# Kernel optimization log

Measured on AMD Instinct MI355X. Metric: run time of the kernel, lower is better.

The kernel has to match this reference:

```python
import jax, jax.numpy as jnp
import numpy as np

B, S, D = 2, 1024, 1024
N_HEADS = 16
R = 128
M = 8
N_NEURONS = 256


def group_gate(gate, n_basis):
    # gate: [B,S,N] -> [B,S,M], sum over consecutive groups, then normalize
    b, s, n = gate.shape
    gs = n // n_basis  # exact by construction (256/8)
    g = gate.reshape(b, s, n_basis, gs).sum(axis=-1)
    return g / (g.sum(axis=-1, keepdims=True) + 1e-8)


def feature_fn(x, neurons, weights):
    # x:[B,S,D], neurons:[M,D,R], weights:[B,S,M] -> h:[B,S,R]
    all_h = jnp.einsum('bsd,mdr->bsmr', x, neurons)
    return jnp.einsum('bsmr,bsm->bsr', all_h, weights)


def restore_fn(h, neurons, weights):
    # h:[B,S,R], neurons:[M,R,D], weights:[B,S,M] -> [B,S,D]
    pre = jnp.einsum('bsr,bsm->bsmr', h, weights)
    return jnp.einsum('bsmr,mrd->bsd', pre, neurons)


def setup_inputs() -> dict:
    key = jax.random.key(0)
    ks = jax.random.split(key, 9)
    sc = 0.02
    return {
        'x': jax.random.normal(ks[0], (B, S, D), jnp.float32),
        'qk_f': jax.random.normal(ks[1], (M, D, R), jnp.float32) * sc,
        'qk_r': jax.random.normal(ks[2], (M, R, D), jnp.float32) * sc,
        'v_f': jax.random.normal(ks[3], (M, D, R), jnp.float32) * sc,
        'v_r': jax.random.normal(ks[4], (M, R, D), jnp.float32) * sc,
        'Wg_q': jax.random.normal(ks[5], (D, N_NEURONS), jnp.float32) * sc,
        'Wg_k': jax.random.normal(ks[6], (D, N_NEURONS), jnp.float32) * sc,
        'Wg_v': jax.random.normal(ks[7], (D, N_NEURONS), jnp.float32) * sc,
        'W_O': jax.random.normal(ks[8], (D, D), jnp.float32) * sc,
    }


def reference(x, qk_f, qk_r, v_f, v_r, Wg_q, Wg_k, Wg_v, W_O):
    # Router gates (softmax over neuron dim), then grouped per basis
    g_Q = jax.nn.softmax(jnp.einsum('bsd,dn->bsn', x, Wg_q), axis=-1)
    g_K = jax.nn.softmax(jnp.einsum('bsd,dn->bsn', x, Wg_k), axis=-1)
    g_V = jax.nn.softmax(jnp.einsum('bsd,dn->bsn', x, Wg_v), axis=-1)
    gQ_b = group_gate(g_Q, M)
    gK_b = group_gate(g_K, M)
    gV_b = group_gate(g_V, M)

    Q = restore_fn(feature_fn(x, qk_f, gQ_b), qk_r, gQ_b)
    K = restore_fn(feature_fn(x, qk_f, gK_b), qk_r, gK_b)
    V = restore_fn(feature_fn(x, v_f, gV_b), v_r, gV_b)

    d_head = D // N_HEADS
    Q = Q.reshape(B, S, N_HEADS, d_head).transpose(0, 2, 1, 3)
    K = K.reshape(B, S, N_HEADS, d_head).transpose(0, 2, 1, 3)
    V = V.reshape(B, S, N_HEADS, d_head).transpose(0, 2, 1, 3)

    scale = jnp.sqrt(jnp.float32(d_head))
    scores = jnp.einsum('bhsd,bhtd->bhst', Q, K) / scale
    causal = jnp.tril(jnp.ones((S, S), dtype=jnp.bool_))
    scores = jnp.where(causal, scores, jnp.finfo(scores.dtype).min)
    attn_w = jax.nn.softmax(scores, axis=-1)
    out = jnp.einsum('bhst,bhtd->bhsd', attn_w, V)
    out = out.transpose(0, 2, 1, 3).reshape(B, S, D)
    out = jnp.einsum('bsd,de->bse', out, W_O)
    return out
```

## Files before the change

### kernel.cpp

```cpp
#include <hip/hip_runtime.h>
#include <hip/hip_bf16.h>

#define BB 2
#define SS 1024
#define DD 1024
#define NH 16
#define DH 64
#define MM 8
#define RR 128
#define NN 256
#define NT (BB*SS)

using bf16 = __hip_bfloat16;

typedef __attribute__((ext_vector_type(8))) short short8;
typedef __attribute__((ext_vector_type(4))) short short4v;
typedef __attribute__((ext_vector_type(4))) float f32x4;

#define EXP2F(x) __builtin_amdgcn_exp2f(x)

#define GLD16(g, l) __builtin_amdgcn_global_load_lds( \
    (const __attribute__((address_space(1))) void*)(g), \
    (__attribute__((address_space(3))) void*)(l), 16, 0, 0)

__device__ __forceinline__ short8 lds_load8(const short* p) {
    short4v a = *(const short4v*)p;
    short4v b = *(const short4v*)(p + 4);
    short8 r;
    r[0] = a[0]; r[1] = a[1]; r[2] = a[2]; r[3] = a[3];
    r[4] = b[0]; r[5] = b[1]; r[6] = b[2]; r[7] = b[3];
    return r;
}

template <int NR>
__device__ __forceinline__ void stage_tile(const bf16* __restrict__ src, int k0,
                                           bf16* lds, int wave, int lane) {
#pragma unroll
    for (int i = 0; i < NR / 32; ++i) {
        const int L = i * 256 + wave * 64 + lane;
        const int row = L >> 3;
        const int gch = (L & 7) ^ ((row >> 1) & 7);
        GLD16(src + (size_t)row * DD + k0 + gch * 8, &lds[(i * 256 + wave * 64) * 8]);
    }
}

__device__ __forceinline__ short8 fragld(const bf16* lds, int rc, int kk, int quad) {
    int slot = (kk * 4 + quad) ^ ((rc >> 1) & 7);
    return *(const short8*)&((const short*)lds)[(rc * 8 + slot) * 8];
}

__device__ __forceinline__ void gemm128_pipe1(
    const bf16* __restrict__ A, const bf16* __restrict__ Bt, bf16* __restrict__ C,
    int Nz, int m0, int n0, bf16* As, bf16* Bs,
    int wave, int lane, int quad, int l15) {
    const int wr = wave >> 1, wc = wave & 1;
    f32x4 acc[4][4];
#pragma unroll
    for (int i = 0; i < 4; ++i)
#pragma unroll
        for (int j = 0; j < 4; ++j) acc[i][j] = (f32x4)0.f;

    const bf16* Ab = A + (size_t)m0 * DD;
    const bf16* Bb = Bt + (size_t)n0 * DD;

    stage_tile<128>(Ab, 0, As, wave, lane);
    stage_tile<128>(Bb, 0, Bs, wave, lane);
    __syncthreads();

    for (int it = 0; it < 16; ++it) {
        const int buf = it & 1;
        const bf16* Asc = As + buf * 8192;
        const bf16* Bsc = Bs + buf * 8192;
        if (it < 15) {
            stage_tile<128>(Ab, (it + 1) * 64, As + (buf ^ 1) * 8192, wave, lane);
            stage_tile<128>(Bb, (it + 1) * 64, Bs + (buf ^ 1) * 8192, wave, lane);
        }
#pragma unroll
        for (int kk = 0; kk < 2; ++kk) {
            short8 aF[4], bF[4];
#pragma unroll
            for (int bi = 0; bi < 4; ++bi) aF[bi] = fragld(Asc, wr * 64 + bi * 16 + l15, kk, quad);
#pragma unroll
            for (int bj = 0; bj < 4; ++bj) bF[bj] = fragld(Bsc, wc * 64 + bj * 16 + l15, kk, quad);
#pragma unroll
            for (int bi = 0; bi < 4; ++bi)
#pragma unroll
                for (int bj = 0; bj < 4; ++bj)
                    acc[bi][bj] = __builtin_amdgcn_mfma_f32_16x16x32_bf16(aF[bi], bF[bj], acc[bi][bj], 0, 0, 0);
        }
        __syncthreads();
    }

#pragma unroll
    for (int bi = 0; bi < 4; ++bi)
#pragma unroll
        for (int bj = 0; bj < 4; ++bj)
#pragma unroll
            for (int r = 0; r < 4; ++r) {
                int row = m0 + wr * 64 + bi * 16 + quad * 4 + r;
                int col = n0 + wc * 64 + bj * 16 + l15;
                C[(size_t)row * Nz + col] = __float2bfloat16(acc[bi][bj][r]);
            }
}

struct ProjArgs {
    const bf16 *xb, *f0, *f1, *wg;
    bf16 *allh0, *allh1, *lg;
    const float* csrc[3];
    bf16* cdst[3];
};

__global__ __launch_bounds__(256, 2) void mfma_proj(ProjArgs P) {
    __shared__ __align__(16) char smem[65536];
    const int bidx = blockIdx.x;
    const int tid = threadIdx.x;

    if (bidx >= 352) {
        float (*tile)[33] = (float(*)[33])smem;
        const int cb = bidx - 352;
        const int j = cb >> 10;
        const int t = cb & 1023;
        const int kb = t >> 5, rb = t & 31;
        const int tx = tid & 31, ty0 = tid >> 5;
        const float* s = P.csrc[j] + ((size_t)(kb * 32) * 1024) + rb * 32 + tx;
#pragma unroll
        for (int p = 0; p < 4; ++p)
            tile[ty0 + p * 8][tx] = s[(size_t)(ty0 + p * 8) * 1024];
        __syncthreads();
        bf16* dd = P.cdst[j] + ((size_t)(rb * 32) * 1024) + kb * 32 + tx;
#pragma unroll
        for (int p = 0; p < 4; ++p)
            dd[(size_t)(ty0 + p * 8) * 1024] = __float2bfloat16(tile[tx][ty0 + p * 8]);
        return;
    }

    bf16* As = (bf16*)smem;
    bf16* Bs = As + 2 * 128 * 64;
    const int wave = tid >> 6, lane = tid & 63;
    const int quad = lane >> 4, l15 = lane & 15;
    const int wk = (bidx & 7) * 44 + (bidx >> 3);
    if (wk < 256) {
        const int z = wk >> 7;
        const int r = wk & 127;
        gemm128_pipe1(P.xb, z ? P.f1 : P.f0, z ? P.allh1 : P.allh0, 1024,
                      (r >> 3) * 128, (r & 7) * 128, As, Bs, wave, lane, quad, l15);
    } else {
        const int r = wk - 256;
        gemm128_pipe1(P.xb, P.wg, P.lg, 768, (r / 6) * 128, (r % 6) * 128,
                      As, Bs, wave, lane, quad, l15);
    }
}

struct RestZ {
    const bf16* A[3];
    const bf16* Bt[3];
    bf16* C[3];
};

__global__ __launch_bounds__(256, 2) void mfma_restore(RestZ R) {
    __shared__ __align__(16) char smem[65536];
    bf16* As = (bf16*)smem;
    bf16* Bs = As + 2 * 128 * 64;
    const int tid = threadIdx.x;
    const int wave = tid >> 6, lane = tid & 63;
    const int quad = lane >> 4, l15 = lane & 15;
    const int wk = (blockIdx.x & 7) * 48 + (blockIdx.x >> 3);
    const int z = wk >> 7;
    const int r = wk & 127;
    gemm128_pipe1(R.A[z], R.Bt[z], R.C[z], DD, (r >> 3) * 128, (r & 7) * 128,
                  As, Bs, wave, lane, quad, l15);
}

__global__ __launch_bounds__(256, 3) void mfma_wo(
    const bf16* __restrict__ A, const bf16* __restrict__ Bt, float* __restrict__ C) {
    __shared__ __align__(16) bf16 As[3 * 64 * 64];
    __shared__ __align__(16) bf16 Bs[3 * 64 * 64];
    const int tid = threadIdx.x;
    const int wave = tid >> 6, lane = tid & 63;
    const int quad = lane >> 4, l15 = lane & 15;
    const int wr = wave >> 1, wc = wave & 1;
    const int wk = (blockIdx.x & 7) * 64 + (blockIdx.x >> 3);
    const int m0 = (wk >> 4) * 64, n0 = (wk & 15) * 64;

    f32x4 acc[2][2];
#pragma unroll
    for (int i = 0; i < 2; ++i)
#pragma unroll
        for (int j = 0; j < 2; ++j) acc[i][j] = (f32x4)0.f;

    const bf16* Ab = A + (size_t)m0 * DD;
    const bf16* Bb = Bt + (size_t)n0 * DD;

    stage_tile<64>(Ab, 0, As, wave, lane);
    stage_tile<64>(Bb, 0, Bs, wave, lane);
    stage_tile<64>(Ab, 64, As + 4096, wave, lane);
    stage_tile<64>(Bb, 64, Bs + 4096, wave, lane);

    int cur = 0;
    for (int it = 0; it < 16; ++it) {
        const int k0 = it * 64;
        int nxt = cur + 2; if (nxt >= 3) nxt -= 3;
        if (it < 14) {
            stage_tile<64>(Ab, k0 + 128, As + nxt * 4096, wave, lane);
            stage_tile<64>(Bb, k0 + 128, Bs + nxt * 4096, wave, lane);
            asm volatile("s_waitcnt vmcnt(8)" ::: "memory");
        } else if (it == 14) {
            asm volatile("s_waitcnt vmcnt(4)" ::: "memory");
        } else {
            asm volatile("s_waitcnt vmcnt(0)" ::: "memory");
        }
        __builtin_amdgcn_s_barrier();

        const bf16* Asc = As + cur * 4096;
        const bf16* Bsc = Bs + cur * 4096;
#pragma unroll
        for (int kk = 0; kk < 2; ++kk) {
            short8 aF[2], bF[2];
#pragma unroll
            for (int bi = 0; bi < 2; ++bi) aF[bi] = fragld(Asc, wr * 32 + bi * 16 + l15, kk, quad);
#pragma unroll
            for (int bj = 0; bj < 2; ++bj) bF[bj] = fragld(Bsc, wc * 32 + bj * 16 + l15, kk, quad);
#pragma unroll
            for (int bi = 0; bi < 2; ++bi)
#pragma unroll
                for (int bj = 0; bj < 2; ++bj)
                    acc[bi][bj] = __builtin_amdgcn_mfma_f32_16x16x32_bf16(aF[bi], bF[bj], acc[bi][bj], 0, 0, 0);
        }
        __builtin_amdgcn_s_barrier();
        cur = cur + 1; if (cur == 3) cur = 0;
    }
#pragma unroll
    for (int bi = 0; bi < 2; ++bi)
#pragma unroll
        for (int bj = 0; bj < 2; ++bj)
#pragma unroll
            for (int r = 0; r < 4; ++r) {
                int row = m0 + wr * 32 + bi * 16 + quad * 4 + r;
                int col = n0 + wc * 32 + bj * 16 + l15;
                C[(size_t)row * DD + col] = acc[bi][bj][r];
            }
}

struct ConvJobs {
    const float* src[9];
    bf16* dst[9];
    int K[9], R[9], G[9];
    int tEnd[9];
};

__global__ void convert_kernel(ConvJobs J) {
    __shared__ float tile[32][33];
    const int b = blockIdx.x;
    int j = 0;
    while (j < 8 && b >= J.tEnd[j]) ++j;
    const int local = b - (j > 0 ? J.tEnd[j - 1] : 0);
    const float* src = J.src[j];
    bf16* dst = J.dst[j];
    const int tid = threadIdx.x;

    if (J.G[j] == 0) {
        size_t base = (size_t)local * 4096 + (size_t)tid * 16;
        const float4* s4 = (const float4*)(src + base);
        short* d = (short*)(dst + base);
#pragma unroll
        for (int c = 0; c < 4; ++c) {
            float4 v = s4[c];
            short4v o;
            bf16 t0 = __float2bfloat16(v.x); o[0] = *(short*)&t0;
            bf16 t1 = __float2bfloat16(v.y); o[1] = *(short*)&t1;
            bf16 t2 = __float2bfloat16(v.z); o[2] = *(short*)&t2;
            bf16 t3 = __float2bfloat16(v.w); o[3] = *(short*)&t3;
            *(short4v*)(d + c * 4) = o;
        }
    } else {
        const int Kj = J.K[j], Rj = J.R[j];
        const int Rb = Rj >> 5, Kb = Kj >> 5;
        const int perG = Kb * Rb;
        const int g = local / perG;
        const int rem = local - g * perG;
        const int kb = rem / Rb, rb = rem - kb * Rb;
        const int tx = tid & 31, ty0 = tid >> 5;
        const float* s = src + ((size_t)(g * Kj + kb * 32) * Rj) + rb * 32 + tx;
#pragma unroll
        for (int p = 0; p < 4; ++p)
            tile[ty0 + p * 8][tx] = s[(size_t)(ty0 + p * 8) * Rj];
        __syncthreads();
        bf16* dd = dst + ((size_t)(g * Rj + rb * 32) * Kj) + kb * 32 + tx;
#pragma unroll
        for (int p = 0; p < 4; ++p)
            dd[(size_t)(ty0 + p * 8) * Kj] = __float2bfloat16(tile[tx][ty0 + p * 8]);
    }
}

__global__ void gate_combine(const bf16* __restrict__ logitsAll,
                             const bf16* __restrict__ allh,
                             bf16* __restrict__ preQ, bf16* __restrict__ preK,
                             bf16* __restrict__ preV) {
    const int t = blockIdx.x;
    const int n = threadIdx.x;
    const int wave = n >> 6, lane = n & 63;
    __shared__ float wred[3][4];
    __shared__ float sred[3][4];
    __shared__ float gred[3][8];

    float v[3], e[3];
#pragma unroll
    for (int z = 0; z < 3; ++z)
        v[z] = __bfloat162float(logitsAll[(size_t)t * 768 + z * 256 + n]);

    float mz[3];
#pragma unroll
    for (int z = 0; z < 3; ++z) {
        mz[z] = v[z];
#pragma unroll
        for (int off = 1; off <= 32; off <<= 1)
            mz[z] = fmaxf(mz[z], __shfl_xor(mz[z], off));
    }
    if (lane == 0) {
#pragma unroll
        for (int z = 0; z < 3; ++z) wred[z][wave] = mz[z];
    }
    __syncthreads();
    float gmax[3];
#pragma unroll
    for (int z = 0; z < 3; ++z)
        gmax[z] = fmaxf(fmaxf(wred[z][0], wred[z][1]), fmaxf(wred[z][2], wred[z][3]));

    float ws[3];
#pragma unroll
    for (int z = 0; z < 3; ++z) {
        e[z] = __expf(v[z] - gmax[z]);
        ws[z] = e[z];
#pragma unroll
        for (int off = 1; off <= 32; off <<= 1)
            ws[z] += __shfl_xor(ws[z], off);
    }
    if (lane == 0) {
#pragma unroll
        for (int z = 0; z < 3; ++z) sred[z][wave] = ws[z];
    }
    float gs[3];
#pragma unroll
    for (int z = 0; z < 3; ++z) {
        gs[z] = e[z];
#pragma unroll
        for (int off = 1; off <= 16; off <<= 1)
            gs[z] += __shfl_xor(gs[z], off);
    }
    __syncthreads();
    float total[3];
#pragma unroll
    for (int z = 0; z < 3; ++z)
        total[z] = sred[z][0] + sred[z][1] + sred[z][2] + sred[z][3];
    if ((n & 31) == 0) {
#pragma unroll
        for (int z = 0; z < 3; ++z) gred[z][n >> 5] = gs[z] / total[z];
    }
    __syncthreads();

    float gv[3][8];
#pragma unroll
    for (int z = 0; z < 3; ++z) {
        float tot = 0.f;
#pragma unroll
        for (int m = 0; m < 8; ++m) tot += gred[z][m];
        float inv = 1.0f / (tot + 1e-8f);
#pragma unroll
        for (int m = 0; m < 8; ++m) gv[z][m] = gred[z][m] * inv;
    }

    const int r0 = n & 127;
    const int half = n >> 7;
    const bf16* src_qk = allh + (size_t)t * 1024;
    const bf16* src_v  = allh + (size_t)NT * DD + (size_t)t * 1024;
    float hq = 0.f, hk = 0.f, hv = 0.f;
#pragma unroll
    for (int m = 0; m < 8; ++m) {
        float aqk = __bfloat162float(src_qk[m * 128 + r0]);
        float av  = __bfloat162float(src_v[m * 128 + r0]);
        hq += aqk * gv[0][m];
        hk += aqk * gv[1][m];
        hv += av  * gv[2][m];
    }
    __syncthreads();
#pragma unroll
    for (int mm = 0; mm < 4; ++mm) {
        int m = half * 4 + mm;
        size_t o = (size_t)t * 1024 + m * 128 + r0;
        preQ[o] = __float2bfloat16(hq * gv[0][m]);
        preK[o] = __float2bfloat16(hk * gv[1][m]);
        preV[o] = __float2bfloat16(hv * gv[2][m]);
    }
}

#define LDK 68

__device__ const int FW24[24] = {
    62, 63, 60, 61, 14,
    58, 59, 56, 12,
    57, 54, 55, 52, 10,
    53, 50, 51, 48, 8,
    49, 6,
    4, 2, 0
};

__global__ __launch_bounds__(256) void flash_attn_hybrid(
    const bf16* __restrict__ Q, const bf16* __restrict__ K,
    const bf16* __restrict__ V, bf16* __restrict__ out,
    float* __restrict__ Opart, float* __restrict__ ml) {
    const int bx = blockIdx.x;
    const int e = FW24[bx >> 5];
    const int bh = bx & 31;
    const int split = e >> 5;
    const int qt = (e >> 1) & 15;
    const int half = e & 1;
    const int h0 = (qt + 2) >> 1;
    const int kt_lo = (split && half) ? h0 : 0;
    const int kt_hi = (split && !half) ? h0 : (qt + 1);
    const int b = bh >> 4;
    const int h = bh & 15;

    const int tid = threadIdx.x;
    const int wave = tid >> 6;
    const int lane = tid & 63;
    const int quad = lane >> 4;
    const int l15 = lane & 15;

    __shared__ short Ks[2][64 * 64];
    __shared__ short Vt[2][64 * LDK];
    __shared__ short Ps[4 * 16 * LDK];

    const int q_row = qt * 64 + wave * 16 + l15;
    const bf16* qptr = Q + (size_t)(b * SS + q_row) * DD + h * DH + quad * 8;
    short8 aq0 = *(const short8*)qptr;
    short8 aq1 = *(const short8*)(qptr + 32);

    const int krp = tid & 31;
    const int dhb = (tid >> 5) * 8;

    float m_r[4], l_r[4];
    f32x4 o[4];
#pragma unroll
    for (int r = 0; r < 4; ++r) { m_r[r] = -3.0e38f; l_r[r] = 0.f; }
#pragma unroll
    for (int cc = 0; cc < 4; ++cc) o[cc] = (f32x4)0.f;

    const float SCL2 = 0.18033688f;

    {
#pragma unroll
        for (int i = 0; i < 2; ++i) {
            const int L = i * 256 + wave * 64 + lane;
            const int row = L >> 3;
            const int gch = (L & 7) ^ ((row >> 1) & 7);
            GLD16(K + (size_t)(b * SS + kt_lo * 64 + row) * DD + h * DH + gch * 8,
                  &Ks[0][(i * 256 + wave * 64) * 8]);
        }
        const bf16* s0 = V + (size_t)(b * SS + kt_lo * 64 + 2 * krp) * DD + h * DH + dhb;
        short8 r0 = *(const short8*)s0;
        short8 r1 = *(const short8*)(s0 + DD);
#pragma unroll
        for (int i = 0; i < 8; ++i) {
            unsigned int pk = (unsigned short)r0[i] | ((unsigned int)(unsigned short)r1[i] << 16);
            *(unsigned int*)&Vt[0][(dhb + i) * LDK + 2 * krp] = pk;
        }
        __syncthreads();
    }

    for (int kt = kt_lo; kt < kt_hi; ++kt) {
        const int buf = (kt - kt_lo) & 1;
        const bool pf = (kt + 1 < kt_hi);
        short8 pr0, pr1;
        if (pf) {
#pragma unroll
            for (int i = 0; i < 2; ++i) {
                const int L = i * 256 + wave * 64 + lane;
                const int row = L >> 3;
                const int gch = (L & 7) ^ ((row >> 1) & 7);
                GLD16(K + (size_t)(b * SS + (kt + 1) * 64 + row) * DD + h * DH + gch * 8,
                      &Ks[buf ^ 1][(i * 256 + wave * 64) * 8]);
            }
            const bf16* s0 = V + (size_t)(b * SS + (kt + 1) * 64 + 2 * krp) * DD + h * DH + dhb;
            pr0 = *(const short8*)s0;
            pr1 = *(const short8*)(s0 + DD);
        }

        const short* KsB = Ks[buf];
        f32x4 s[4];
#pragma unroll
        for (int cc = 0; cc < 4; ++cc) {
            int n = cc * 16 + l15;
            int sl0 = quad ^ ((n >> 1) & 7);
            int sl1 = (quad + 4) ^ ((n >> 1) & 7);
            short8 bk0 = *(const short8*)&KsB[(n * 8 + sl0) * 8];
            short8 bk1 = *(const short8*)&KsB[(n * 8 + sl1) * 8];
            f32x4 acc = (f32x4)0.f;
            acc = __builtin_amdgcn_mfma_f32_16x16x32_bf16(aq0, bk0, acc, 0, 0, 0);
            acc = __builtin_amdgcn_mfma_f32_16x16x32_bf16(aq1, bk1, acc, 0, 0, 0);
            s[cc] = acc;
        }

        const bool diag = (kt == qt);
#pragma unroll
        for (int cc = 0; cc < 4; ++cc) {
#pragma unroll
            for (int r = 0; r < 4; ++r) {
                float v = s[cc][r] * SCL2;
                if (diag) {
                    int row_rel = wave * 16 + quad * 4 + r;
                    int col_rel = cc * 16 + l15;
                    if (col_rel > row_rel) v = -3.0e38f;
                }
                s[cc][r] = v;
            }
        }

        float mx[4];
#pragma unroll
        for (int r = 0; r < 4; ++r) {
            float m2 = fmaxf(fmaxf(s[0][r], s[1][r]), fmaxf(s[2][r], s[3][r]));
            m2 = fmaxf(m2, __shfl_xor(m2, 1));
            m2 = fmaxf(m2, __shfl_xor(m2, 2));
            m2 = fmaxf(m2, __shfl_xor(m2, 4));
            m2 = fmaxf(m2, __shfl_xor(m2, 8));
            mx[r] = m2;
        }
        bool grew = false;
#pragma unroll
        for (int r = 0; r < 4; ++r) grew = grew || (mx[r] > m_r[r] + 8.f);
        float alpha[4];
        const bool need = __any(grew);
        if (need) {
#pragma unroll
            for (int r = 0; r < 4; ++r) {
                float nm = fmaxf(m_r[r], mx[r]);
                alpha[r] = EXP2F(m_r[r] - nm);
                m_r[r] = nm;
            }
        }

        float p[4][4];
#pragma unroll
        for (int r = 0; r < 4; ++r) {
            float rs = 0.f;
#pragma unroll
            for (int cc = 0; cc < 4; ++cc) {
                float e2 = EXP2F(s[cc][r] - m_r[r]);
                p[cc][r] = e2;
                rs += e2;
            }
            rs += __shfl_xor(rs, 1);
            rs += __shfl_xor(rs, 2);
            rs += __shfl_xor(rs, 4);
            rs += __shfl_xor(rs, 8);
            if (need) l_r[r] = l_r[r] * alpha[r] + rs;
            else      l_r[r] += rs;
        }
        if (need) {
#pragma unroll
            for (int cc = 0; cc < 4; ++cc)
#pragma unroll
                for (int r = 0; r < 4; ++r) o[cc][r] *= alpha[r];
        }

        short* pw = &Ps[wave * 16 * LDK];
#pragma unroll
        for (int cc = 0; cc < 4; ++cc)
#pragma unroll
            for (int r = 0; r < 4; ++r) {
                bf16 hb = __float2bfloat16(p[cc][r]);
                pw[(quad * 4 + r) * LDK + cc * 16 + l15] = *(short*)&hb;
            }

        short8 ap0 = lds_load8(&pw[l15 * LDK + quad * 8]);
        short8 ap1 = lds_load8(&pw[l15 * LDK + 32 + quad * 8]);

        const short* VtB = Vt[buf];
#pragma unroll
        for (int cc = 0; cc < 4; ++cc) {
            short8 bv0 = lds_load8(&VtB[(cc * 16 + l15) * LDK + quad * 8]);
            short8 bv1 = lds_load8(&VtB[(cc * 16 + l15) * LDK + 32 + quad * 8]);
            o[cc] = __builtin_amdgcn_mfma_f32_16x16x32_bf16(ap0, bv0, o[cc], 0, 0, 0);
            o[cc] = __builtin_amdgcn_mfma_f32_16x16x32_bf16(ap1, bv1, o[cc], 0, 0, 0);
        }

        if (pf) {
#pragma unroll
            for (int i = 0; i < 8; ++i) {
                unsigned int pk = (unsigned short)pr0[i] | ((unsigned int)(unsigned short)pr1[i] << 16);
                *(unsigned int*)&Vt[buf ^ 1][(dhb + i) * LDK + 2 * krp] = pk;
            }
        }
        __syncthreads();
    }

    if (!split) {
        float inv[4];
#pragma unroll
        for (int r = 0; r < 4; ++r) inv[r] = 1.0f / l_r[r];
#pragma unroll
        for (int cc = 0; cc < 4; ++cc)
#pragma unroll
            for (int r = 0; r < 4; ++r) {
                int row = qt * 64 + wave * 16 + quad * 4 + r;
                out[(size_t)(b * SS + row) * DD + h * DH + cc * 16 + l15] =
                    __float2bfloat16(o[cc][r] * inv[r]);
            }
    } else {
        const int idx = (bh * 8 + (qt - 8)) * 2 + half;
        float* ob = Opart + (size_t)idx * 4096;
#pragma unroll
        for (int cc = 0; cc < 4; ++cc)
#pragma unroll
            for (int r = 0; r < 4; ++r) {
                int row = wave * 16 + quad * 4 + r;
                ob[row * 64 + cc * 16 + l15] = o[cc][r];
            }
        if (l15 == 0) {
#pragma unroll
            for (int r = 0; r < 4; ++r) {
                int row = wave * 16 + quad * 4 + r;
                ml[(size_t)idx * 128 + row] = m_r[r];
                ml[(size_t)idx * 128 + 64 + row] = l_r[r];
            }
        }
    }
}

__global__ void attn_combine(const float* __restrict__ Opart,
                             const float* __restrict__ ml,
                             bf16* __restrict__ out) {
    const int bidx = blockIdx.x;
    const int bh = bidx & 31;
    const int qt = (bidx >> 5) + 8;
    const int b = bh >> 4;
    const int h = bh & 15;
    const int tid = threadIdx.x;
    const int row = tid >> 2;
    const int cg = tid & 3;

    const int p0 = (bh * 8 + (qt - 8)) * 2;
    const int p1 = p0 + 1;
    float m0 = ml[(size_t)p0 * 128 + row], l0 = ml[(size_t)p0 * 128 + 64 + row];
    float m1 = ml[(size_t)p1 * 128 + row], l1 = ml[(size_t)p1 * 128 + 64 + row];
    float ms = fmaxf(m0, m1);
    float w0 = EXP2F(m0 - ms), w1 = EXP2F(m1 - ms);
    float inv = 1.0f / (l0 * w0 + l1 * w1);

    const float* o0 = Opart + (size_t)p0 * 4096 + row * 64 + cg * 16;
    const float* o1 = Opart + (size_t)p1 * 4096 + row * 64 + cg * 16;
    short out16[16];
#pragma unroll
    for (int j = 0; j < 16; j += 4) {
        float4 a = *(const float4*)(o0 + j);
        float4 bb = *(const float4*)(o1 + j);
        bf16 t0 = __float2bfloat16((a.x * w0 + bb.x * w1) * inv); out16[j] = *(short*)&t0;
        bf16 t1 = __float2bfloat16((a.y * w0 + bb.y * w1) * inv); out16[j + 1] = *(short*)&t1;
        bf16 t2 = __float2bfloat16((a.z * w0 + bb.z * w1) * inv); out16[j + 2] = *(short*)&t2;
        bf16 t3 = __float2bfloat16((a.w * w0 + bb.w * w1) * inv); out16[j + 3] = *(short*)&t3;
    }
    short* dst = (short*)(out + (size_t)(b * SS + qt * 64 + row) * DD + h * DH + cg * 16);
    *(short8*)dst = *(short8*)&out16[0];
    *(short8*)(dst + 8) = *(short8*)&out16[8];
}

extern "C" void kernel_launch(void* const* d_in, const int* in_sizes, int n_in,
                              void* d_out, int out_size, void* d_ws, size_t ws_size,
                              hipStream_t stream) {
    const float* x    = (const float*)d_in[0];
    const float* qk_f = (const float*)d_in[1];
    const float* qk_r = (const float*)d_in[2];
    const float* v_f  = (const float*)d_in[3];
    const float* v_r  = (const float*)d_in[4];
    const float* Wg_q = (const float*)d_in[5];
    const float* Wg_k = (const float*)d_in[6];
    const float* Wg_v = (const float*)d_in[7];
    const float* W_O  = (const float*)d_in[8];

    char* w = (char*)d_ws;
    const size_t MB = 1 << 20;
    bf16* xb     = (bf16*)(w + 0);
    bf16* wg_bt  = (bf16*)(w + 4 * MB);
    bf16* fbt    = (bf16*)(w + (size_t)(5.5 * MB));
    bf16* logits = (bf16*)(w + (size_t)(9.5 * MB));
    bf16* qkr_bt = (bf16*)(w + 16 * MB);
    bf16* vr_bt  = (bf16*)(w + 18 * MB);
    bf16* wo_bt  = (bf16*)(w + 20 * MB);
    bf16* preQ   = (bf16*)(w + 0);
    bf16* preK   = (bf16*)(w + 4 * MB);
    bf16* Kb     = (bf16*)(w + 8 * MB);
    bf16* Vb     = (bf16*)(w + 12 * MB);
    bf16* attnb  = (bf16*)(w + 0);
    float* Opart = (float*)(w + 32 * MB);
    float* mlbuf = (float*)(w + 48 * MB);
    bf16* allh   = (bf16*)d_out;
    bf16* preV   = allh + (size_t)NT * DD;
    bf16* Qb     = (bf16*)d_out;
    float* out   = (float*)d_out;

    ConvJobs J;
    J.src[0] = x;    J.dst[0] = xb;               J.K[0] = 0;    J.R[0] = 0;    J.G[0] = 0;
    J.src[1] = qk_f; J.dst[1] = fbt;              J.K[1] = 1024; J.R[1] = 128;  J.G[1] = 8;
    J.src[2] = v_f;  J.dst[2] = fbt + 1024*1024;  J.K[2] = 1024; J.R[2] = 128;  J.G[2] = 8;
    J.src[3] = Wg_q; J.dst[3] = wg_bt;            J.K[3] = 1024; J.R[3] = 256;  J.G[3] = 1;
    J.src[4] = Wg_k; J.dst[4] = wg_bt + 256*1024; J.K[4] = 1024; J.R[4] = 256;  J.G[4] = 1;
    J.src[5] = Wg_v; J.dst[5] = wg_bt + 2*256*1024; J.K[5] = 1024; J.R[5] = 256; J.G[5] = 1;
    int tiles[6] = {512, 1024, 1024, 256, 256, 256};
    int cum = 0;
    for (int i = 0; i < 6; ++i) { cum += tiles[i]; J.tEnd[i] = cum; }
    for (int i = 6; i < 9; ++i) { J.tEnd[i] = cum; J.src[i] = nullptr; J.dst[i] = nullptr; J.K[i] = J.R[i] = J.G[i] = 0; }
    convert_kernel<<<cum, 256, 0, stream>>>(J);

    ProjArgs Pp;
    Pp.xb = xb; Pp.f0 = fbt; Pp.f1 = fbt + 1024*1024; Pp.wg = wg_bt;
    Pp.allh0 = allh; Pp.allh1 = allh + (size_t)NT * DD; Pp.lg = logits;
    Pp.csrc[0] = qk_r; Pp.csrc[1] = v_r; Pp.csrc[2] = W_O;
    Pp.cdst[0] = qkr_bt; Pp.cdst[1] = vr_bt; Pp.cdst[2] = wo_bt;
    mfma_proj<<<dim3(3424), 256, 0, stream>>>(Pp);

    gate_combine<<<NT, 256, 0, stream>>>(logits, allh, preQ, preK, preV);

    RestZ Pr;
    Pr.A[0] = preQ; Pr.A[1] = preK; Pr.A[2] = preV;
    Pr.Bt[0] = qkr_bt; Pr.Bt[1] = qkr_bt; Pr.Bt[2] = vr_bt;
    Pr.C[0] = Qb; Pr.C[1] = Kb; Pr.C[2] = Vb;
    mfma_restore<<<dim3(384), 256, 0, stream>>>(Pr);

    flash_attn_hybrid<<<dim3(768), 256, 0, stream>>>(Qb, Kb, Vb, attnb, Opart, mlbuf);

    attn_combine<<<dim3(256), 256, 0, stream>>>(Opart, mlbuf, attnb);

    mfma_wo<<<dim3(512), 256, 0, stream>>>(attnb, wo_bt, out);
}
```

Baseline: 172.9 us.

## Fuse split-KV attention combine into the output projection GEMM

Removes the separate attn_combine kernel. For the later query tiles (qt >= 8), the W_O GEMM now builds its A operand directly from the two partial attention outputs: it computes per-row merge weights from the stored m/l values, blends the fp32 partials, converts them to bf16 in registers and writes them into LDS. Earlier tiles keep the previous triple-buffered async load path. This saves one launch and the bf16 write and reread of the combined rows, but the fused blocks read twice as much fp32 data and use a plain double buffer with register staging, which may run slower per block.

```diff
diff --git a/kernel.cpp b/kernel.cpp
--- a/kernel.cpp
+++ b/kernel.cpp
@@ -172,15 +172,17 @@
 }
 
 __global__ __launch_bounds__(256, 3) void mfma_wo(
-    const bf16* __restrict__ A, const bf16* __restrict__ Bt, float* __restrict__ C) {
-    __shared__ __align__(16) bf16 As[3 * 64 * 64];
-    __shared__ __align__(16) bf16 Bs[3 * 64 * 64];
+    const bf16* __restrict__ A, const bf16* __restrict__ Bt, float* __restrict__ C,
+    const float* __restrict__ Opart, const float* __restrict__ ml) {
+    __shared__ __align__(16) char smem[49152];
     const int tid = threadIdx.x;
     const int wave = tid >> 6, lane = tid & 63;
     const int quad = lane >> 4, l15 = lane & 15;
     const int wr = wave >> 1, wc = wave & 1;
     const int wk = (blockIdx.x & 7) * 64 + (blockIdx.x >> 3);
     const int m0 = (wk >> 4) * 64, n0 = (wk & 15) * 64;
+    const int qt = (m0 >> 6) & 15;
+    const int b = m0 >> 10;
 
     f32x4 acc[2][2];
 #pragma unroll
@@ -188,47 +190,139 @@
 #pragma unroll
         for (int j = 0; j < 2; ++j) acc[i][j] = (f32x4)0.f;
 
-    const bf16* Ab = A + (size_t)m0 * DD;
     const bf16* Bb = Bt + (size_t)n0 * DD;
 
-    stage_tile<64>(Ab, 0, As, wave, lane);
-    stage_tile<64>(Bb, 0, Bs, wave, lane);
-    stage_tile<64>(Ab, 64, As + 4096, wave, lane);
-    stage_tile<64>(Bb, 64, Bs + 4096, wave, lane);
-
-    int cur = 0;
-    for (int it = 0; it < 16; ++it) {
-        const int k0 = it * 64;
-        int nxt = cur + 2; if (nxt >= 3) nxt -= 3;
-        if (it < 14) {
-            stage_tile<64>(Ab, k0 + 128, As + nxt * 4096, wave, lane);
-            stage_tile<64>(Bb, k0 + 128, Bs + nxt * 4096, wave, lane);
-            asm volatile("s_waitcnt vmcnt(8)" ::: "memory");
-        } else if (it == 14) {
-            asm volatile("s_waitcnt vmcnt(4)" ::: "memory");
-        } else {
-            asm volatile("s_waitcnt vmcnt(0)" ::: "memory");
-        }
-        __builtin_amdgcn_s_barrier();
-
-        const bf16* Asc = As + cur * 4096;
-        const bf16* Bsc = Bs + cur * 4096;
-#pragma unroll
-        for (int kk = 0; kk < 2; ++kk) {
-            short8 aF[2], bF[2];
-#pragma unroll
-            for (int bi = 0; bi < 2; ++bi) aF[bi] = fragld(Asc, wr * 32 + bi * 16 + l15, kk, quad);
-#pragma unroll
-            for (int bj = 0; bj < 2; ++bj) bF[bj] = fragld(Bsc, wc * 32 + bj * 16 + l15, kk, quad);
-#pragma unroll
-            for (int bi = 0; bi < 2; ++bi)
-#pragma unroll
-                for (int bj = 0; bj < 2; ++bj)
-                    acc[bi][bj] = __builtin_amdgcn_mfma_f32_16x16x32_bf16(aF[bi], bF[bj], acc[bi][bj], 0, 0, 0);
-        }
-        __builtin_amdgcn_s_barrier();
-        cur = cur + 1; if (cur == 3) cur = 0;
-    }
+    if (qt < 8) {
+        bf16* As = (bf16*)smem;
+        bf16* Bs = As + 3 * 4096;
+        const bf16* Ab = A + (size_t)m0 * DD;
+
+        stage_tile<64>(Ab, 0, As, wave, lane);
+        stage_tile<64>(Bb, 0, Bs, wave, lane);
+        stage_tile<64>(Ab, 64, As + 4096, wave, lane);
+        stage_tile<64>(Bb, 64, Bs + 4096, wave, lane);
+
+        int cur = 0;
+        for (int it = 0; it < 16; ++it) {
+            const int k0 = it * 64;
+            int nxt = cur + 2; if (nxt >= 3) nxt -= 3;
+            if (it < 14) {
+                stage_tile<64>(Ab, k0 + 128, As + nxt * 4096, wave, lane);
+                stage_tile<64>(Bb, k0 + 128, Bs + nxt * 4096, wave, lane);
+                asm volatile("s_waitcnt vmcnt(8)" ::: "memory");
+            } else if (it == 14) {
+                asm volatile("s_waitcnt vmcnt(4)" ::: "memory");
+            } else {
+                asm volatile("s_waitcnt vmcnt(0)" ::: "memory");
+            }
+            __builtin_amdgcn_s_barrier();
+
+            const bf16* Asc = As + cur * 4096;
+            const bf16* Bsc = Bs + cur * 4096;
+#pragma unroll
+            for (int kk = 0; kk < 2; ++kk) {
+                short8 aF[2], bF[2];
+#pragma unroll
+                for (int bi = 0; bi < 2; ++bi) aF[bi] = fragld(Asc, wr * 32 + bi * 16 + l15, kk, quad);
+#pragma unroll
+                for (int bj = 0; bj < 2; ++bj) bF[bj] = fragld(Bsc, wc * 32 + bj * 16 + l15, kk, quad);
+#pragma unroll
+                for (int bi = 0; bi < 2; ++bi)
+#pragma unroll
+                    for (int bj = 0; bj < 2; ++bj)
+                        acc[bi][bj] = __builtin_amdgcn_mfma_f32_16x16x32_bf16(aF[bi], bF[bj], acc[bi][bj], 0, 0, 0);
+            }
+            __builtin_amdgcn_s_barrier();
+            cur = cur + 1; if (cur == 3) cur = 0;
+        }
+    } else {
+        bf16* As2 = (bf16*)smem;
+        bf16* Bs2 = As2 + 2 * 4096;
+        float* wA = (float*)(smem + 32768);
+        float* wB = wA + 1024;
+
+        const int base = b * 256 + (qt - 8) * 2;
+        for (int p = tid; p < 1024; p += 256) {
+            const int hh = p >> 6, row = p & 63;
+            const int idx = base + hh * 16;
+            float m0v = ml[(size_t)idx * 128 + row];
+            float l0v = ml[(size_t)idx * 128 + 64 + row];
+            float m1v = ml[(size_t)(idx + 1) * 128 + row];
+            float l1v = ml[(size_t)(idx + 1) * 128 + 64 + row];
+            float ms = fmaxf(m0v, m1v);
+            float w0 = EXP2F(m0v - ms), w1 = EXP2F(m1v - ms);
+            float inv = 1.0f / (l0v * w0 + l1v * w1);
+            wA[hh * 64 + row] = w0 * inv;
+            wB[hh * 64 + row] = w1 * inv;
+        }
+
+        float4 rg[8];
+        auto loadA = [&](int h) {
+            const float* o0 = Opart + (size_t)(base + h * 16) * 4096;
+            const float* o1 = o0 + 4096;
+#pragma unroll
+            for (int u = 0; u < 2; ++u) {
+                const int L = tid + u * 256;
+                const int row = L >> 3;
+                const int gch = (L & 7) ^ ((row >> 1) & 7);
+                const float* p0 = o0 + row * 64 + gch * 8;
+                const float* p1 = o1 + row * 64 + gch * 8;
+                rg[u * 4 + 0] = *(const float4*)p0;
+                rg[u * 4 + 1] = *(const float4*)(p0 + 4);
+                rg[u * 4 + 2] = *(const float4*)p1;
+                rg[u * 4 + 3] = *(const float4*)(p1 + 4);
+            }
+        };
+        auto writeA = [&](int h, bf16* dst) {
+#pragma unroll
+            for (int u = 0; u < 2; ++u) {
+                const int L = tid + u * 256;
+                const int row = L >> 3;
+                const float wa = wA[h * 64 + row], wb = wB[h * 64 + row];
+                short8 o8;
+#pragma unroll
+                for (int j = 0; j < 4; ++j) {
+                    float v0 = (&rg[u * 4 + 0].x)[j] * wa + (&rg[u * 4 + 2].x)[j] * wb;
+                    float v1 = (&rg[u * 4 + 1].x)[j] * wa + (&rg[u * 4 + 3].x)[j] * wb;
+                    bf16 t0 = __float2bfloat16(v0); o8[j] = *(short*)&t0;
+                    bf16 t1 = __float2bfloat16(v1); o8[4 + j] = *(short*)&t1;
+                }
+                *(short8*)&((short*)dst)[L * 8] = o8;
+            }
+        };
+
+        __syncthreads();
+        loadA(0);
+        stage_tile<64>(Bb, 0, Bs2, wave, lane);
+        writeA(0, As2);
+        __syncthreads();
+
+        for (int it = 0; it < 16; ++it) {
+            const int buf = it & 1;
+            if (it < 15) {
+                loadA(it + 1);
+                stage_tile<64>(Bb, (it + 1) * 64, Bs2 + (buf ^ 1) * 4096, wave, lane);
+            }
+            const bf16* Asc = As2 + buf * 4096;
+            const bf16* Bsc = Bs2 + buf * 4096;
+#pragma unroll
+            for (int kk = 0; kk < 2; ++kk) {
+                short8 aF[2], bF[2];
+#pragma unroll
+                for (int bi = 0; bi < 2; ++bi) aF[bi] = fragld(Asc, wr * 32 + bi * 16 + l15, kk, quad);
+#pragma unroll
+                for (int bj = 0; bj < 2; ++bj) bF[bj] = fragld(Bsc, wc * 32 + bj * 16 + l15, kk, quad);
+#pragma unroll
+                for (int bi = 0; bi < 2; ++bi)
+#pragma unroll
+                    for (int bj = 0; bj < 2; ++bj)
+                        acc[bi][bj] = __builtin_amdgcn_mfma_f32_16x16x32_bf16(aF[bi], bF[bj], acc[bi][bj], 0, 0, 0);
+            }
+            if (it < 15) writeA(it + 1, As2 + (buf ^ 1) * 4096);
+            __syncthreads();
+        }
+    }
+
 #pragma unroll
     for (int bi = 0; bi < 2; ++bi)
 #pragma unroll
@@ -625,43 +719,6 @@
             }
         }
     }
-}
-
-__global__ void attn_combine(const float* __restrict__ Opart,
-                             const float* __restrict__ ml,
-                             bf16* __restrict__ out) {
-    const int bidx = blockIdx.x;
-    const int bh = bidx & 31;
-    const int qt = (bidx >> 5) + 8;
-    const int b = bh >> 4;
-    const int h = bh & 15;
-    const int tid = threadIdx.x;
-    const int row = tid >> 2;
-    const int cg = tid & 3;
-
-    const int p0 = (bh * 8 + (qt - 8)) * 2;
-    const int p1 = p0 + 1;
-    float m0 = ml[(size_t)p0 * 128 + row], l0 = ml[(size_t)p0 * 128 + 64 + row];
-    float m1 = ml[(size_t)p1 * 128 + row], l1 = ml[(size_t)p1 * 128 + 64 + row];
-    float ms = fmaxf(m0, m1);
-    float w0 = EXP2F(m0 - ms), w1 = EXP2F(m1 - ms);
-    float inv = 1.0f / (l0 * w0 + l1 * w1);
-
-    const float* o0 = Opart + (size_t)p0 * 4096 + row * 64 + cg * 16;
-    const float* o1 = Opart + (size_t)p1 * 4096 + row * 64 + cg * 16;
-    short out16[16];
-#pragma unroll
-    for (int j = 0; j < 16; j += 4) {
-        float4 a = *(const float4*)(o0 + j);
-        float4 bb = *(const float4*)(o1 + j);
-        bf16 t0 = __float2bfloat16((a.x * w0 + bb.x * w1) * inv); out16[j] = *(short*)&t0;
-        bf16 t1 = __float2bfloat16((a.y * w0 + bb.y * w1) * inv); out16[j + 1] = *(short*)&t1;
-        bf16 t2 = __float2bfloat16((a.z * w0 + bb.z * w1) * inv); out16[j + 2] = *(short*)&t2;
-        bf16 t3 = __float2bfloat16((a.w * w0 + bb.w * w1) * inv); out16[j + 3] = *(short*)&t3;
-    }
-    short* dst = (short*)(out + (size_t)(b * SS + qt * 64 + row) * DD + h * DH + cg * 16);
-    *(short8*)dst = *(short8*)&out16[0];
-    *(short8*)(dst + 8) = *(short8*)&out16[8];
 }
 
 extern "C" void kernel_launch(void* const* d_in, const int* in_sizes, int n_in,
@@ -728,7 +785,5 @@
 
     flash_attn_hybrid<<<dim3(768), 256, 0, stream>>>(Qb, Kb, Vb, attnb, Opart, mlbuf);
 
-    attn_combine<<<dim3(256), 256, 0, stream>>>(Opart, mlbuf, attnb);
-
-    mfma_wo<<<dim3(512), 256, 0, stream>>>(attnb, wo_bt, out);
-}
+    mfma_wo<<<dim3(512), 256, 0, stream>>>(attnb, wo_bt, out, Opart, mlbuf);
+}
```

Measured after the change: 177.0 us. +2.4%, slower.

## Fuse split-KV attention combine into flash kernel via atomic last-arriver merge

Applied to the files above, without the earlier changes.

Removes the separate attn_combine launch. Each split half writes its partial O, m and l, fences, and bumps a per-pair atomic counter. The second block to arrive reads the other half's partials and writes the merged bf16 output. The counters are zeroed by block 0 of the preceding restore kernel. This saves a kernel launch and one read of its own partial, at the cost of extra fences and atomics and a serialized merge tail inside the attention kernel.

```diff
diff --git a/kernel.cpp b/kernel.cpp
--- a/kernel.cpp
+++ b/kernel.cpp
@@ -157,11 +157,12 @@
     bf16* C[3];
 };
 
-__global__ __launch_bounds__(256, 2) void mfma_restore(RestZ R) {
+__global__ __launch_bounds__(256, 2) void mfma_restore(RestZ R, int* cnt) {
     __shared__ __align__(16) char smem[65536];
     bf16* As = (bf16*)smem;
     bf16* Bs = As + 2 * 128 * 64;
     const int tid = threadIdx.x;
+    if (blockIdx.x == 0) cnt[tid] = 0;
     const int wave = tid >> 6, lane = tid & 63;
     const int quad = lane >> 4, l15 = lane & 15;
     const int wk = (blockIdx.x & 7) * 48 + (blockIdx.x >> 3);
@@ -407,7 +408,7 @@
 __global__ __launch_bounds__(256) void flash_attn_hybrid(
     const bf16* __restrict__ Q, const bf16* __restrict__ K,
     const bf16* __restrict__ V, bf16* __restrict__ out,
-    float* __restrict__ Opart, float* __restrict__ ml) {
+    float* __restrict__ Opart, float* __restrict__ ml, int* __restrict__ cnt) {
     const int bx = blockIdx.x;
     const int e = FW24[bx >> 5];
     const int bh = bx & 31;
@@ -429,6 +430,7 @@
     __shared__ short Ks[2][64 * 64];
     __shared__ short Vt[2][64 * LDK];
     __shared__ short Ps[4 * 16 * LDK];
+    __shared__ int tick;
 
     const int q_row = qt * 64 + wave * 16 + l15;
     const bf16* qptr = Q + (size_t)(b * SS + q_row) * DD + h * DH + quad * 8;
@@ -607,7 +609,8 @@
                     __float2bfloat16(o[cc][r] * inv[r]);
             }
     } else {
-        const int idx = (bh * 8 + (qt - 8)) * 2 + half;
+        const int pairIdx = bh * 8 + (qt - 8);
+        const int idx = pairIdx * 2 + half;
         float* ob = Opart + (size_t)idx * 4096;
 #pragma unroll
         for (int cc = 0; cc < 4; ++cc)
@@ -624,44 +627,39 @@
                 ml[(size_t)idx * 128 + 64 + row] = l_r[r];
             }
         }
-    }
-}
-
-__global__ void attn_combine(const float* __restrict__ Opart,
-                             const float* __restrict__ ml,
-                             bf16* __restrict__ out) {
-    const int bidx = blockIdx.x;
-    const int bh = bidx & 31;
-    const int qt = (bidx >> 5) + 8;
-    const int b = bh >> 4;
-    const int h = bh & 15;
-    const int tid = threadIdx.x;
-    const int row = tid >> 2;
-    const int cg = tid & 3;
-
-    const int p0 = (bh * 8 + (qt - 8)) * 2;
-    const int p1 = p0 + 1;
-    float m0 = ml[(size_t)p0 * 128 + row], l0 = ml[(size_t)p0 * 128 + 64 + row];
-    float m1 = ml[(size_t)p1 * 128 + row], l1 = ml[(size_t)p1 * 128 + 64 + row];
-    float ms = fmaxf(m0, m1);
-    float w0 = EXP2F(m0 - ms), w1 = EXP2F(m1 - ms);
-    float inv = 1.0f / (l0 * w0 + l1 * w1);
-
-    const float* o0 = Opart + (size_t)p0 * 4096 + row * 64 + cg * 16;
-    const float* o1 = Opart + (size_t)p1 * 4096 + row * 64 + cg * 16;
-    short out16[16];
-#pragma unroll
-    for (int j = 0; j < 16; j += 4) {
-        float4 a = *(const float4*)(o0 + j);
-        float4 bb = *(const float4*)(o1 + j);
-        bf16 t0 = __float2bfloat16((a.x * w0 + bb.x * w1) * inv); out16[j] = *(short*)&t0;
-        bf16 t1 = __float2bfloat16((a.y * w0 + bb.y * w1) * inv); out16[j + 1] = *(short*)&t1;
-        bf16 t2 = __float2bfloat16((a.z * w0 + bb.z * w1) * inv); out16[j + 2] = *(short*)&t2;
-        bf16 t3 = __float2bfloat16((a.w * w0 + bb.w * w1) * inv); out16[j + 3] = *(short*)&t3;
-    }
-    short* dst = (short*)(out + (size_t)(b * SS + qt * 64 + row) * DD + h * DH + cg * 16);
-    *(short8*)dst = *(short8*)&out16[0];
-    *(short8*)(dst + 8) = *(short8*)&out16[8];
+
+        __threadfence();
+        __syncthreads();
+        if (tid == 0) tick = atomicAdd(&cnt[pairIdx], 1);
+        __syncthreads();
+        if (tick == 1) {
+            __threadfence();
+            const int other = pairIdx * 2 + (half ^ 1);
+            const float* o1b = Opart + (size_t)other * 4096;
+            float w0[4], w1[4], inv[4];
+#pragma unroll
+            for (int r = 0; r < 4; ++r) {
+                int row = wave * 16 + quad * 4 + r;
+                float m1 = ml[(size_t)other * 128 + row];
+                float l1 = ml[(size_t)other * 128 + 64 + row];
+                float ms = fmaxf(m_r[r], m1);
+                w0[r] = EXP2F(m_r[r] - ms);
+                w1[r] = EXP2F(m1 - ms);
+                inv[r] = 1.0f / (l_r[r] * w0[r] + l1 * w1[r]);
+            }
+#pragma unroll
+            for (int cc = 0; cc < 4; ++cc)
+#pragma unroll
+                for (int r = 0; r < 4; ++r) {
+                    int row = wave * 16 + quad * 4 + r;
+                    float ov = o1b[row * 64 + cc * 16 + l15];
+                    float v = (o[cc][r] * w0[r] + ov * w1[r]) * inv[r];
+                    int grow = qt * 64 + row;
+                    out[(size_t)(b * SS + grow) * DD + h * DH + cc * 16 + l15] =
+                        __float2bfloat16(v);
+                }
+        }
+    }
 }
 
 extern "C" void kernel_launch(void* const* d_in, const int* in_sizes, int n_in,
@@ -693,6 +691,7 @@
     bf16* attnb  = (bf16*)(w + 0);
     float* Opart = (float*)(w + 32 * MB);
     float* mlbuf = (float*)(w + 48 * MB);
+    int*   cnt   = (int*)(w + 49 * MB);
     bf16* allh   = (bf16*)d_out;
     bf16* preV   = allh + (size_t)NT * DD;
     bf16* Qb     = (bf16*)d_out;
@@ -724,11 +723,10 @@
     Pr.A[0] = preQ; Pr.A[1] = preK; Pr.A[2] = preV;
     Pr.Bt[0] = qkr_bt; Pr.Bt[1] = qkr_bt; Pr.Bt[2] = vr_bt;
     Pr.C[0] = Qb; Pr.C[1] = Kb; Pr.C[2] = Vb;
-    mfma_restore<<<dim3(384), 256, 0, stream>>>(Pr);
-
-    flash_attn_hybrid<<<dim3(768), 256, 0, stream>>>(Qb, Kb, Vb, attnb, Opart, mlbuf);
-
-    attn_combine<<<dim3(256), 256, 0, stream>>>(Opart, mlbuf, attnb);
+    mfma_restore<<<dim3(384), 256, 0, stream>>>(Pr, cnt);
+
+    flash_attn_hybrid<<<dim3(768), 256, 0, stream>>>(Qb, Kb, Vb, attnb,
+                                                     Opart, mlbuf, cnt);
 
     mfma_wo<<<dim3(512), 256, 0, stream>>>(attnb, wo_bt, out);
 }
```

After: 259.1 us. +49.9%, slower.
